# Kernel tuning notes

Hardware: AMD Instinct MI355X
Metric: run time of the kernel (lower is better)

## Reference

```python
import jax, jax.numpy as jnp
import numpy as np

N = 20000      # nodes
E = 160000     # edges
F_IN = 64      # node_feature_dim
HID = 256      # hidden_dim (= per-head out_channels, concat=False)
HEADS = 4
OUT = 2
BN_EPS = 1e-5


def setup_inputs() -> dict:
    key = jax.random.key(0)
    ks = jax.random.split(key, 24)
    s = 0.02

    def w(k, shape):
        return jax.random.normal(k, shape, jnp.float32) * s

    return {
        "node_feature": jax.random.normal(ks[0], (N, F_IN), jnp.float32),
        "edge_index": jax.random.randint(ks[1], (2, E), 0, N, jnp.int32),
        # layer 1 (in=F_IN)
        "wq1": w(ks[2], (F_IN, HEADS * HID)), "bq1": w(ks[3], (HEADS * HID,)),
        "wk1": w(ks[4], (F_IN, HEADS * HID)), "bk1": w(ks[5], (HEADS * HID,)),
        "wv1": w(ks[6], (F_IN, HEADS * HID)), "bv1": w(ks[7], (HEADS * HID,)),
        "ws1": w(ks[8], (F_IN, HID)),        "bs1": w(ks[9], (HID,)),
        # layer 2 (in=HID)
        "wq2": w(ks[10], (HID, HEADS * HID)), "bq2": w(ks[11], (HEADS * HID,)),
        "wk2": w(ks[12], (HID, HEADS * HID)), "bk2": w(ks[13], (HEADS * HID,)),
        "wv2": w(ks[14], (HID, HEADS * HID)), "bv2": w(ks[15], (HEADS * HID,)),
        "ws2": w(ks[16], (HID, HID)),         "bs2": w(ks[17], (HID,)),
        # batch norm affine
        "bn_gamma": jnp.ones((HID,), jnp.float32) + w(ks[18], (HID,)),
        "bn_beta": w(ks[19], (HID,)),
        # final linear
        "lin_w": w(ks[20], (HID, OUT)), "lin_b": w(ks[21], (OUT,)),
    }


def _transformer_conv(x, src, dst, wq, bq, wk, bk, wv, bv, ws, bs):
    """PyG TransformerConv, heads=HEADS, concat=False (mean over heads), root_weight."""
    n = x.shape[0]
    q = (x @ wq + bq).reshape(n, HEADS, HID)   # [N,H,C]
    k = (x @ wk + bk).reshape(n, HEADS, HID)
    v = (x @ wv + bv).reshape(n, HEADS, HID)
    # per-edge attention logits: q_i . k_j / sqrt(C)   (message j->i, i = dst)
    alpha = jnp.einsum('ehc,ehc->eh', q[dst], k[src]) / jnp.sqrt(jnp.float32(HID))  # [E,H]
    # scatter-softmax over incoming edges of each target node
    m = jax.ops.segment_max(alpha, dst, num_segments=n)
    m = jnp.where(jnp.isfinite(m), m, 0.0)  # nodes with no in-edges
    ex = jnp.exp(alpha - m[dst])
    denom = jax.ops.segment_sum(ex, dst, num_segments=n)
    a = ex / (denom[dst] + 1e-16)                          # [E,H]
    out = jax.ops.segment_sum(v[src] * a[..., None], dst, num_segments=n)  # [N,H,C]
    return out.mean(axis=1) + x @ ws + bs                  # concat=False -> head mean; + skip


def reference(node_feature, edge_index,
              wq1, bq1, wk1, bk1, wv1, bv1, ws1, bs1,
              wq2, bq2, wk2, bk2, wv2, bv2, ws2, bs2,
              bn_gamma, bn_beta, lin_w, lin_b):
    src, dst = edge_index[0], edge_index[1]
    x = _transformer_conv(node_feature, src, dst, wq1, bq1, wk1, bk1, wv1, bv1, ws1, bs1)
    x = _transformer_conv(x, src, dst, wq2, bq2, wk2, bk2, wv2, bv2, ws2, bs2)
    # BatchNorm1d (training mode: batch statistics, biased variance)
    mu = x.mean(axis=0)
    var = jnp.mean(jnp.square(x - mu), axis=0)
    x = bn_gamma * (x - mu) / jnp.sqrt(var + BN_EPS) + bn_beta
    rsu_embedding = x[0:1]                     # [1, HID]
    logits = jax.nn.relu(x @ lin_w + lin_b)    # [N, OUT]
    action_prob = jax.nn.softmax(logits, axis=1)
    return (action_prob, rsu_embedding)
```

## Files before the change

kernel.cpp:

```cpp
#include <hip/hip_runtime.h>
#include <hip/hip_bf16.h>
#include <math.h>

#define DI __device__ __forceinline__

constexpr int NN   = 20000;
constexpr int NE   = 160000;
constexpr int FIN  = 64;
constexpr int HIDC = 256;
constexpr int NH   = 4;
constexpr int NOUT = 3328;
constexpr int QKVW = 3072;
constexpr int CAPD = 128;

typedef __attribute__((ext_vector_type(8))) short short8;
typedef __attribute__((ext_vector_type(4))) float f32x4;
typedef __attribute__((ext_vector_type(2))) float f32x2;

DI float bf2f(unsigned short u) { return __uint_as_float(((unsigned)u) << 16); }

DI void gld16(const void* g, void* l) {
  __builtin_amdgcn_global_load_lds((const __attribute__((address_space(1))) unsigned*)g,
                                   (__attribute__((address_space(3))) unsigned*)l, 16, 0, 0);
}

DI unsigned fp8pack4(float a, float b, float c, float d) {
  int v = __builtin_amdgcn_cvt_pk_fp8_f32(a, b, 0, false);
  v = __builtin_amdgcn_cvt_pk_fp8_f32(c, d, v, true);
  return (unsigned)v;
}

__global__ void k_count(const int* __restrict__ dst, int* __restrict__ deg, int e_) {
  int e = blockIdx.x * blockDim.x + threadIdx.x;
  if (e < e_) atomicAdd(&deg[dst[e]], 1);
}

__global__ void k_scan(const int* __restrict__ deg, int* __restrict__ offs,
                       int* __restrict__ cursor, int n_) {
  __shared__ int part[1024];
  int tid = threadIdx.x;
  const int CH = (n_ + 1023) >> 10;
  int base = tid * CH;
  int s = 0;
  for (int i = 0; i < CH; ++i) { int idx = base + i; if (idx < n_) s += deg[idx]; }
  part[tid] = s;
  __syncthreads();
  for (int off = 1; off < 1024; off <<= 1) {
    int v = (tid >= off) ? part[tid - off] : 0;
    __syncthreads();
    part[tid] += v;
    __syncthreads();
  }
  int run = (tid == 0) ? 0 : part[tid - 1];
  for (int i = 0; i < CH; ++i) {
    int idx = base + i;
    if (idx < n_) { offs[idx] = run; cursor[idx] = run; run += deg[idx]; }
  }
  if (tid == 1023) offs[n_] = run;
}

__global__ void k_scatter(const int* __restrict__ dst, int* __restrict__ cursor,
                          int* __restrict__ eid, int e_) {
  int e = blockIdx.x * blockDim.x + threadIdx.x;
  if (e < e_) {
    int p = atomicAdd(&cursor[dst[e]], 1);
    eid[p] = e;
  }
}

__global__ void k_cast(const float* __restrict__ x, __hip_bfloat16* __restrict__ xb, int n) {
  int i = blockIdx.x * 256 + threadIdx.x;
  if (i < n) xb[i] = __float2bfloat16(x[i]);
}

template <int K>
__global__ void k_pack(const float* __restrict__ wq, const float* __restrict__ bq,
                       const float* __restrict__ wk, const float* __restrict__ bk,
                       const float* __restrict__ wv, const float* __restrict__ bv,
                       const float* __restrict__ ws, const float* __restrict__ bs,
                       __hip_bfloat16* __restrict__ Wt, float* __restrict__ biasp) {
  int n = blockIdx.x * 128 + threadIdx.x;
  int k = blockIdx.y;
  const float* w; const float* b; int off; int M;
  if (n < 1024)      { w = wq; b = bq; off = n;        M = 1024; }
  else if (n < 2048) { w = wk; b = bk; off = n - 1024; M = 1024; }
  else if (n < 3072) { w = wv; b = bv; off = n - 2048; M = 1024; }
  else               { w = ws; b = bs; off = n - 3072; M = 256;  }
  Wt[(size_t)n * K + k] = __float2bfloat16(w[(size_t)k * M + off]);
  if (k == 0) biasp[n] = b[off];
}

template <int K>
__global__ __launch_bounds__(256) void k_gemm_mfma(
    const __hip_bfloat16* __restrict__ X, const __hip_bfloat16* __restrict__ Wt,
    const float* __restrict__ biasp,
    __hip_bfloat16* __restrict__ qb, unsigned char* __restrict__ kb,
    unsigned char* __restrict__ vb, float* __restrict__ skip, int nrows,
    int RB, int CB) {
  __shared__ char lds[36864];
  const int tid = threadIdx.x;

  const int nwg = RB * CB;
  int bid = blockIdx.x;
  {
    int q8 = nwg >> 3, r8 = nwg & 7;
    int xcd = bid & 7, idx = bid >> 3;
    bid = (xcd < r8 ? xcd * (q8 + 1) : r8 * (q8 + 1) + (xcd - r8) * q8) + idx;
  }
  const int bm = (bid / CB) * 128;
  const int bn = (bid % CB) * 128;
  constexpr int KT = K / 32;

  const int srow = tid & 127;
  int ar = bm + srow; if (ar >= nrows) ar = nrows - 1;
  const int br = bn + srow;
  const int kb0 = (tid >> 7) * 8;
  const __hip_bfloat16* ax = X + (size_t)ar * K + kb0;
  const __hip_bfloat16* bx = Wt + (size_t)br * K + kb0;

  const int l = tid & 63, w = tid >> 6;
  const int wr = w >> 1, wc = w & 1;
  const int lm = l & 15, lk = l >> 4;
  const int aoff = (lk * 128 + wr * 64 + lm) * 16;
  const int boff = 8192 + (lk * 128 + wc * 64 + lm) * 16;

  f32x4 acc[4][4] = {};

  auto STAGE = [&](int buf, int kt) {
    char* base = lds + buf * 16384;
    const int ko = kt * 32;
    gld16(ax + ko,      base + tid * 16);
    gld16(ax + ko + 16, base + 4096 + tid * 16);
    gld16(bx + ko,      base + 8192 + tid * 16);
    gld16(bx + ko + 16, base + 12288 + tid * 16);
  };

  int cur = 0;
  STAGE(0, 0);
  __syncthreads();
#pragma unroll
  for (int kt = 0; kt < KT; ++kt) {
    if (kt + 1 < KT) STAGE(cur ^ 1, kt + 1);
    const char* base = lds + cur * 16384;
    short8 a[4], b[4];
#pragma unroll
    for (int m = 0; m < 4; ++m) a[m] = *(const short8*)(base + aoff + m * 256);
#pragma unroll
    for (int n = 0; n < 4; ++n) b[n] = *(const short8*)(base + boff + n * 256);
#pragma unroll
    for (int m = 0; m < 4; ++m)
#pragma unroll
      for (int n = 0; n < 4; ++n)
        acc[m][n] = __builtin_amdgcn_mfma_f32_16x16x32_bf16(a[m], b[n], acc[m][n], 0, 0, 0);
    __syncthreads();
    cur ^= 1;
  }

  if (bn < QKVW) {
    char* wb = lds + w * 9216;
    float bia[4];
#pragma unroll
    for (int n = 0; n < 4; ++n) bia[n] = biasp[bn + wc * 64 + n * 16 + lm];
#pragma unroll
    for (int m = 0; m < 4; ++m)
#pragma unroll
      for (int n = 0; n < 4; ++n)
#pragma unroll
        for (int r = 0; r < 4; ++r) {
          int rl = m * 16 + lk * 4 + r;
          int cl = n * 16 + lm;
          *(__hip_bfloat16*)(wb + rl * 144 + cl * 2) = __float2bfloat16(acc[m][n][r] + bia[n]);
        }
    __syncthreads();
    const int c8 = l & 7;
    const int r8 = l >> 3;
#pragma unroll
    for (int it = 0; it < 8; ++it) {
      int rl = it * 8 + r8;
      int grow = bm + wr * 64 + rl;
      if (grow >= nrows) continue;
      short8 t = *(const short8*)(wb + rl * 144 + c8 * 16);
      if (bn < 1024) {
        int col = bn + wc * 64 + c8 * 8;
        *(short8*)(qb + (size_t)grow * 1024 + col) = t;
      } else {
        float f0 = bf2f((unsigned short)t[0]), f1 = bf2f((unsigned short)t[1]);
        float f2 = bf2f((unsigned short)t[2]), f3 = bf2f((unsigned short)t[3]);
        float f4 = bf2f((unsigned short)t[4]), f5 = bf2f((unsigned short)t[5]);
        float f6 = bf2f((unsigned short)t[6]), f7 = bf2f((unsigned short)t[7]);
        uint2 d;
        d.x = fp8pack4(f0, f1, f2, f3);
        d.y = fp8pack4(f4, f5, f6, f7);
        if (bn < 2048) {
          int col = bn - 1024 + wc * 64 + c8 * 8;
          *(uint2*)(kb + (size_t)grow * 1024 + col) = d;
        } else {
          int col = bn - 2048 + wc * 64 + c8 * 8;
          *(uint2*)(vb + (size_t)grow * 1024 + col) = d;
        }
      }
    }
  } else {
    const int rbase = bm + wr * 64 + lk * 4;
    const int cb = bn + wc * 64 + lm;
#pragma unroll
    for (int n = 0; n < 4; ++n) {
      int col = cb + n * 16;
      float bia = biasp[col];
      int sc = col - QKVW;
#pragma unroll
      for (int m = 0; m < 4; ++m)
#pragma unroll
        for (int r = 0; r < 4; ++r) {
          int rr = rbase + m * 16 + r;
          if (rr < nrows) skip[(size_t)rr * HIDC + sc] = acc[m][n][r] + bia;
        }
    }
  }
}

__global__ __launch_bounds__(256) void k_attn(
    const __hip_bfloat16* __restrict__ qb, const unsigned char* __restrict__ kb,
    const unsigned char* __restrict__ vb,
    const int* __restrict__ offs, const int* __restrict__ eid,
    const int* __restrict__ src, float* __restrict__ xio,
    __hip_bfloat16* __restrict__ xb) {
  int n = blockIdx.x;
  int s0 = offs[n], s1 = offs[n + 1];
  int deg = s1 - s0;
  int tid = threadIdx.x;
  if (deg == 0) {
    if (xb != nullptr && tid < 64) {
      int c = tid * 4;
      const float* xr = xio + (size_t)n * HIDC;
#pragma unroll
      for (int j = 0; j < 4; ++j) xb[(size_t)n * HIDC + c + j] = __float2bfloat16(xr[c + j]);
    }
    return;
  }
  __shared__ int ses[CAPD];
  __shared__ float red[NH][HIDC];
  int h = tid >> 6, lane = tid & 63;
  int dc = deg < CAPD ? deg : CAPD;
  for (int i = tid; i < dc; i += 256) ses[i] = src[eid[s0 + i]];
  __syncthreads();

  const int hc = h * HIDC;
  int c = lane * 4;
  ushort4 q4 = *(const ushort4*)((const ushort*)qb + (size_t)n * 1024 + hc + c);
  float qx = bf2f(q4.x), qy = bf2f(q4.y), qz = bf2f(q4.z), qw = bf2f(q4.w);

  float denom = 0.f;
  float4 acc = make_float4(0.f, 0.f, 0.f, 0.f);
  for (int i = 0; i < deg; ++i) {
    int s = (i < CAPD) ? ses[i] : src[eid[s0 + i]];
    unsigned ku = *(const unsigned*)(kb + (size_t)s * 1024 + hc + c);
    unsigned vu = *(const unsigned*)(vb + (size_t)s * 1024 + hc + c);
    f32x2 k01 = __builtin_amdgcn_cvt_pk_f32_fp8(ku, false);
    f32x2 k23 = __builtin_amdgcn_cvt_pk_f32_fp8(ku, true);
    float p = qx * k01.x + qy * k01.y + qz * k23.x + qw * k23.y;
#pragma unroll
    for (int off = 32; off > 0; off >>= 1) p += __shfl_xor(p, off);
    float wgt = __expf(p * 0.0625f);
    denom += wgt;
    f32x2 v01 = __builtin_amdgcn_cvt_pk_f32_fp8(vu, false);
    f32x2 v23 = __builtin_amdgcn_cvt_pk_f32_fp8(vu, true);
    acc.x = fmaf(wgt, v01.x, acc.x);
    acc.y = fmaf(wgt, v01.y, acc.y);
    acc.z = fmaf(wgt, v23.x, acc.z);
    acc.w = fmaf(wgt, v23.y, acc.w);
  }
  float dinv = 1.f / (denom + 1e-16f);
  red[h][c + 0] = acc.x * dinv;
  red[h][c + 1] = acc.y * dinv;
  red[h][c + 2] = acc.z * dinv;
  red[h][c + 3] = acc.w * dinv;
  __syncthreads();
  if (tid < 64) {
    int c0 = tid * 4;
    float* xr = xio + (size_t)n * HIDC;
#pragma unroll
    for (int j = 0; j < 4; ++j) {
      float m = (red[0][c0 + j] + red[1][c0 + j] + red[2][c0 + j] + red[3][c0 + j]) * 0.25f;
      float val = m + xr[c0 + j];
      xr[c0 + j] = val;
      if (xb != nullptr) xb[(size_t)n * HIDC + c0 + j] = __float2bfloat16(val);
    }
  }
}

__global__ void k_bnstats(const float* __restrict__ x, float* __restrict__ sums,
                          float* __restrict__ sumsq, int n_) {
  int t = threadIdx.x;
  float s = 0.f, s2 = 0.f;
  for (int r = blockIdx.x; r < n_; r += gridDim.x) {
    float vv = x[(size_t)r * HIDC + t];
    s += vv; s2 += vv * vv;
  }
  atomicAdd(&sums[t], s);
  atomicAdd(&sumsq[t], s2);
}

__global__ void k_bnfin(const float* __restrict__ sums, const float* __restrict__ sumsq,
                        float* __restrict__ mu, float* __restrict__ rinv, int n_) {
  int t = threadIdx.x;
  float m = sums[t] / n_;
  float va = sumsq[t] / n_ - m * m;
  mu[t] = m;
  rinv[t] = 1.f / sqrtf(fmaxf(va, 0.f) + 1e-5f);
}

__global__ __launch_bounds__(64) void k_final(
    const float* __restrict__ x, const float* __restrict__ mu, const float* __restrict__ rinv,
    const float* __restrict__ gamma, const float* __restrict__ beta,
    const float* __restrict__ lw, const float* __restrict__ lb,
    float* __restrict__ out, int n_) {
  int n = blockIdx.x;
  int lane = threadIdx.x;
  int c = lane * 4;
  const float* xr = x + (size_t)n * HIDC;
  float4 xv = *(const float4*)(xr + c);
  float4 muv = *(const float4*)(mu + c);
  float4 rv  = *(const float4*)(rinv + c);
  float4 gv  = *(const float4*)(gamma + c);
  float4 bv  = *(const float4*)(beta + c);
  float y0 = gv.x * (xv.x - muv.x) * rv.x + bv.x;
  float y1 = gv.y * (xv.y - muv.y) * rv.y + bv.y;
  float y2 = gv.z * (xv.z - muv.z) * rv.z + bv.z;
  float y3 = gv.w * (xv.w - muv.w) * rv.w + bv.w;
  float4 wa = *(const float4*)(lw + (size_t)c * 2);
  float4 wb = *(const float4*)(lw + (size_t)c * 2 + 4);
  float p0 = y0 * wa.x + y1 * wa.z + y2 * wb.x + y3 * wb.z;
  float p1 = y0 * wa.y + y1 * wa.w + y2 * wb.y + y3 * wb.w;
#pragma unroll
  for (int off = 32; off > 0; off >>= 1) {
    p0 += __shfl_xor(p0, off);
    p1 += __shfl_xor(p1, off);
  }
  if (n == 0) *(float4*)(out + (size_t)NN * 2 + c) = make_float4(y0, y1, y2, y3);
  if (lane == 0) {
    float l0 = fmaxf(p0 + lb[0], 0.f);
    float l1 = fmaxf(p1 + lb[1], 0.f);
    float m = fmaxf(l0, l1);
    float e0 = expf(l0 - m), e1 = expf(l1 - m);
    float inv = 1.f / (e0 + e1);
    out[(size_t)n * 2 + 0] = e0 * inv;
    out[(size_t)n * 2 + 1] = e1 * inv;
  }
}

extern "C" void kernel_launch(void* const* d_in, const int* in_sizes, int n_in,
                              void* d_out, int out_size, void* d_ws, size_t ws_size,
                              hipStream_t stream) {
  const float* x0  = (const float*)d_in[0];
  const int*   ei  = (const int*)d_in[1];
  const float* wq1 = (const float*)d_in[2];  const float* bq1 = (const float*)d_in[3];
  const float* wk1 = (const float*)d_in[4];  const float* bk1 = (const float*)d_in[5];
  const float* wv1 = (const float*)d_in[6];  const float* bv1 = (const float*)d_in[7];
  const float* ws1 = (const float*)d_in[8];  const float* bs1 = (const float*)d_in[9];
  const float* wq2 = (const float*)d_in[10]; const float* bq2 = (const float*)d_in[11];
  const float* wk2 = (const float*)d_in[12]; const float* bk2 = (const float*)d_in[13];
  const float* wv2 = (const float*)d_in[14]; const float* bv2 = (const float*)d_in[15];
  const float* ws2 = (const float*)d_in[16]; const float* bs2 = (const float*)d_in[17];
  const float* gam = (const float*)d_in[18]; const float* bet = (const float*)d_in[19];
  const float* lw  = (const float*)d_in[20]; const float* lb  = (const float*)d_in[21];
  const int* srcv = ei;
  const int* dstv = ei + NE;

  char* p = (char*)d_ws;
  auto take = [&](size_t bytes) {
    char* r = p;
    p += (bytes + 255) & ~(size_t)255;
    return r;
  };
  __hip_bfloat16* qb = (__hip_bfloat16*)take((size_t)NN * 1024 * 2);
  unsigned char* kbuf = (unsigned char*)take((size_t)NN * 1024);
  unsigned char* vbuf = (unsigned char*)take((size_t)NN * 1024);
  __hip_bfloat16* x0b = (__hip_bfloat16*)take((size_t)NN * FIN * 2);
  __hip_bfloat16* x2b = (__hip_bfloat16*)take((size_t)NN * HIDC * 2);
  __hip_bfloat16* Wt  = (__hip_bfloat16*)take((size_t)NOUT * HIDC * 2);
  float* x2    = (float*)take((size_t)NN * HIDC * 4);
  float* x3    = (float*)take((size_t)NN * HIDC * 4);
  float* biasp = (float*)take((size_t)NOUT * 4);
  float* bnbuf = (float*)take(4 * HIDC * 4);
  int* deg    = (int*)take((size_t)NN * 4);
  int* offs   = (int*)take((size_t)(NN + 1) * 4);
  int* cursor = (int*)take((size_t)NN * 4);
  int* eidb   = (int*)take((size_t)NE * 4);
  if ((size_t)(p - (char*)d_ws) > ws_size) return;

  float* sums  = bnbuf;
  float* sumsq = bnbuf + HIDC;
  float* mu    = bnbuf + 2 * HIDC;
  float* rinv  = bnbuf + 3 * HIDC;

  hipMemsetAsync(deg, 0, (size_t)NN * 4, stream);
  hipMemsetAsync(bnbuf, 0, 2 * HIDC * 4, stream);
  k_count<<<(NE + 255) / 256, 256, 0, stream>>>(dstv, deg, NE);
  k_scan<<<1, 1024, 0, stream>>>(deg, offs, cursor, NN);
  k_scatter<<<(NE + 255) / 256, 256, 0, stream>>>(dstv, cursor, eidb, NE);
  k_cast<<<(NN * FIN + 255) / 256, 256, 0, stream>>>(x0, x0b, NN * FIN);

  const int RB = (NN + 127) / 128;
  const int CB = NOUT / 128;
  k_pack<FIN><<<dim3(CB, FIN), 128, 0, stream>>>(wq1, bq1, wk1, bk1, wv1, bv1, ws1, bs1, Wt, biasp);
  k_gemm_mfma<FIN><<<RB * CB, 256, 0, stream>>>(x0b, Wt, biasp, qb, kbuf, vbuf, x2, NN, RB, CB);
  k_attn<<<NN, 256, 0, stream>>>(qb, kbuf, vbuf, offs, eidb, srcv, x2, x2b);
  k_pack<HIDC><<<dim3(CB, HIDC), 128, 0, stream>>>(wq2, bq2, wk2, bk2, wv2, bv2, ws2, bs2, Wt, biasp);
  k_gemm_mfma<HIDC><<<RB * CB, 256, 0, stream>>>(x2b, Wt, biasp, qb, kbuf, vbuf, x3, NN, RB, CB);
  k_attn<<<NN, 256, 0, stream>>>(qb, kbuf, vbuf, offs, eidb, srcv, x3, nullptr);
  k_bnstats<<<256, 256, 0, stream>>>(x3, sums, sumsq, NN);
  k_bnfin<<<1, HIDC, 0, stream>>>(sums, sumsq, mu, rinv, NN);
  k_final<<<NN, 64, 0, stream>>>(x3, mu, rinv, gam, bet, lw, lb, (float*)d_out, NN);
}
```

Before: 413.5 us.

## Load GEMM operands directly to registers, store Q in fp8, fuse small kernels

```diff
diff --git a/kernel.cpp b/kernel.cpp
--- a/kernel.cpp
+++ b/kernel.cpp
@@ -10,7 +10,6 @@
 constexpr int HIDC = 256;
 constexpr int NH   = 4;
 constexpr int NOUT = 3328;
-constexpr int QKVW = 3072;
 constexpr int CAPD = 128;
 
 typedef __attribute__((ext_vector_type(8))) short short8;
@@ -18,11 +17,6 @@
 typedef __attribute__((ext_vector_type(2))) float f32x2;
 
 DI float bf2f(unsigned short u) { return __uint_as_float(((unsigned)u) << 16); }
-
-DI void gld16(const void* g, void* l) {
-  __builtin_amdgcn_global_load_lds((const __attribute__((address_space(1))) unsigned*)g,
-                                   (__attribute__((address_space(3))) unsigned*)l, 16, 0, 0);
-}
 
 DI unsigned fp8pack4(float a, float b, float c, float d) {
   int v = __builtin_amdgcn_cvt_pk_fp8_f32(a, b, 0, false);
@@ -30,9 +24,11 @@
   return (unsigned)v;
 }
 
-__global__ void k_count(const int* __restrict__ dst, int* __restrict__ deg, int e_) {
-  int e = blockIdx.x * blockDim.x + threadIdx.x;
-  if (e < e_) atomicAdd(&deg[dst[e]], 1);
+__global__ void k_prep(const float* __restrict__ x, __hip_bfloat16* __restrict__ xb,
+                       const int* __restrict__ dst, int* __restrict__ deg) {
+  int gid = blockIdx.x * 256 + threadIdx.x;
+  if (gid < NN * FIN) xb[gid] = __float2bfloat16(x[gid]);
+  if (gid < NE) atomicAdd(&deg[dst[gid]], 1);
 }
 
 __global__ void k_scan(const int* __restrict__ deg, int* __restrict__ offs,
@@ -68,11 +64,6 @@
   }
 }
 
-__global__ void k_cast(const float* __restrict__ x, __hip_bfloat16* __restrict__ xb, int n) {
-  int i = blockIdx.x * 256 + threadIdx.x;
-  if (i < n) xb[i] = __float2bfloat16(x[i]);
-}
-
 template <int K>
 __global__ void k_pack(const float* __restrict__ wq, const float* __restrict__ bq,
                        const float* __restrict__ wk, const float* __restrict__ bk,
@@ -91,13 +82,13 @@
 }
 
 template <int K>
-__global__ __launch_bounds__(256) void k_gemm_mfma(
+__global__ __launch_bounds__(256) void k_gemm_reg(
     const __hip_bfloat16* __restrict__ X, const __hip_bfloat16* __restrict__ Wt,
     const float* __restrict__ biasp,
-    __hip_bfloat16* __restrict__ qb, unsigned char* __restrict__ kb,
-    unsigned char* __restrict__ vb, float* __restrict__ skip, int nrows,
-    int RB, int CB) {
-  __shared__ char lds[36864];
+    unsigned char* __restrict__ qb, unsigned char* __restrict__ kb,
+    unsigned char* __restrict__ vb, __hip_bfloat16* __restrict__ skipb,
+    int nrows, int RB, int CB) {
+  __shared__ char eplds[36864];
   const int tid = threadIdx.x;
 
   const int nwg = RB * CB;
@@ -111,130 +102,98 @@
   const int bn = (bid % CB) * 128;
   constexpr int KT = K / 32;
 
-  const int srow = tid & 127;
-  int ar = bm + srow; if (ar >= nrows) ar = nrows - 1;
-  const int br = bn + srow;
-  const int kb0 = (tid >> 7) * 8;
-  const __hip_bfloat16* ax = X + (size_t)ar * K + kb0;
-  const __hip_bfloat16* bx = Wt + (size_t)br * K + kb0;
-
   const int l = tid & 63, w = tid >> 6;
   const int wr = w >> 1, wc = w & 1;
   const int lm = l & 15, lk = l >> 4;
-  const int aoff = (lk * 128 + wr * 64 + lm) * 16;
-  const int boff = 8192 + (lk * 128 + wc * 64 + lm) * 16;
+
+  const __hip_bfloat16* Ap[4];
+  const __hip_bfloat16* Bp[4];
+#pragma unroll
+  for (int m = 0; m < 4; ++m) {
+    int row = bm + wr * 64 + m * 16 + lm;
+    if (row >= nrows) row = nrows - 1;
+    Ap[m] = X + (size_t)row * K + lk * 8;
+  }
+#pragma unroll
+  for (int n = 0; n < 4; ++n) {
+    int col = bn + wc * 64 + n * 16 + lm;
+    Bp[n] = Wt + (size_t)col * K + lk * 8;
+  }
 
   f32x4 acc[4][4] = {};
-
-  auto STAGE = [&](int buf, int kt) {
-    char* base = lds + buf * 16384;
-    const int ko = kt * 32;
-    gld16(ax + ko,      base + tid * 16);
-    gld16(ax + ko + 16, base + 4096 + tid * 16);
-    gld16(bx + ko,      base + 8192 + tid * 16);
-    gld16(bx + ko + 16, base + 12288 + tid * 16);
-  };
-
-  int cur = 0;
-  STAGE(0, 0);
-  __syncthreads();
-#pragma unroll
+#pragma unroll 2
   for (int kt = 0; kt < KT; ++kt) {
-    if (kt + 1 < KT) STAGE(cur ^ 1, kt + 1);
-    const char* base = lds + cur * 16384;
     short8 a[4], b[4];
 #pragma unroll
-    for (int m = 0; m < 4; ++m) a[m] = *(const short8*)(base + aoff + m * 256);
-#pragma unroll
-    for (int n = 0; n < 4; ++n) b[n] = *(const short8*)(base + boff + n * 256);
+    for (int m = 0; m < 4; ++m) a[m] = *(const short8*)(Ap[m] + kt * 32);
+#pragma unroll
+    for (int n = 0; n < 4; ++n) b[n] = *(const short8*)(Bp[n] + kt * 32);
 #pragma unroll
     for (int m = 0; m < 4; ++m)
 #pragma unroll
       for (int n = 0; n < 4; ++n)
         acc[m][n] = __builtin_amdgcn_mfma_f32_16x16x32_bf16(a[m], b[n], acc[m][n], 0, 0, 0);
-    __syncthreads();
-    cur ^= 1;
-  }
-
-  if (bn < QKVW) {
-    char* wb = lds + w * 9216;
-    float bia[4];
-#pragma unroll
-    for (int n = 0; n < 4; ++n) bia[n] = biasp[bn + wc * 64 + n * 16 + lm];
-#pragma unroll
-    for (int m = 0; m < 4; ++m)
-#pragma unroll
-      for (int n = 0; n < 4; ++n)
-#pragma unroll
-        for (int r = 0; r < 4; ++r) {
-          int rl = m * 16 + lk * 4 + r;
-          int cl = n * 16 + lm;
-          *(__hip_bfloat16*)(wb + rl * 144 + cl * 2) = __float2bfloat16(acc[m][n][r] + bia[n]);
-        }
-    __syncthreads();
-    const int c8 = l & 7;
-    const int r8 = l >> 3;
-#pragma unroll
-    for (int it = 0; it < 8; ++it) {
-      int rl = it * 8 + r8;
-      int grow = bm + wr * 64 + rl;
-      if (grow >= nrows) continue;
-      short8 t = *(const short8*)(wb + rl * 144 + c8 * 16);
-      if (bn < 1024) {
-        int col = bn + wc * 64 + c8 * 8;
-        *(short8*)(qb + (size_t)grow * 1024 + col) = t;
-      } else {
-        float f0 = bf2f((unsigned short)t[0]), f1 = bf2f((unsigned short)t[1]);
-        float f2 = bf2f((unsigned short)t[2]), f3 = bf2f((unsigned short)t[3]);
-        float f4 = bf2f((unsigned short)t[4]), f5 = bf2f((unsigned short)t[5]);
-        float f6 = bf2f((unsigned short)t[6]), f7 = bf2f((unsigned short)t[7]);
-        uint2 d;
-        d.x = fp8pack4(f0, f1, f2, f3);
-        d.y = fp8pack4(f4, f5, f6, f7);
-        if (bn < 2048) {
-          int col = bn - 1024 + wc * 64 + c8 * 8;
-          *(uint2*)(kb + (size_t)grow * 1024 + col) = d;
-        } else {
-          int col = bn - 2048 + wc * 64 + c8 * 8;
-          *(uint2*)(vb + (size_t)grow * 1024 + col) = d;
-        }
+  }
+
+  char* ep = eplds + w * 9216;
+  float bia[4];
+#pragma unroll
+  for (int n = 0; n < 4; ++n) bia[n] = biasp[bn + wc * 64 + n * 16 + lm];
+#pragma unroll
+  for (int m = 0; m < 4; ++m)
+#pragma unroll
+    for (int n = 0; n < 4; ++n)
+#pragma unroll
+      for (int r = 0; r < 4; ++r) {
+        int rl = m * 16 + lk * 4 + r;
+        int cl = n * 16 + lm;
+        *(__hip_bfloat16*)(ep + rl * 144 + cl * 2) = __float2bfloat16(acc[m][n][r] + bia[n]);
       }
+  const int c8 = l & 7;
+  const int r8 = l >> 3;
+#pragma unroll
+  for (int it = 0; it < 8; ++it) {
+    int rl = it * 8 + r8;
+    int grow = bm + wr * 64 + rl;
+    if (grow >= nrows) continue;
+    short8 t = *(const short8*)(ep + rl * 144 + c8 * 16);
+    int colg = bn + wc * 64 + c8 * 8;
+    if (colg < 3072) {
+      float f0 = bf2f((unsigned short)t[0]), f1 = bf2f((unsigned short)t[1]);
+      float f2 = bf2f((unsigned short)t[2]), f3 = bf2f((unsigned short)t[3]);
+      float f4 = bf2f((unsigned short)t[4]), f5 = bf2f((unsigned short)t[5]);
+      float f6 = bf2f((unsigned short)t[6]), f7 = bf2f((unsigned short)t[7]);
+      uint2 d;
+      d.x = fp8pack4(f0, f1, f2, f3);
+      d.y = fp8pack4(f4, f5, f6, f7);
+      if (colg < 1024)      *(uint2*)(qb + (size_t)grow * 1024 + colg)        = d;
+      else if (colg < 2048) *(uint2*)(kb + (size_t)grow * 1024 + colg - 1024) = d;
+      else                  *(uint2*)(vb + (size_t)grow * 1024 + colg - 2048) = d;
+    } else {
+      *(short8*)((__hip_bfloat16*)skipb + (size_t)grow * HIDC + colg - 3072) = t;
     }
-  } else {
-    const int rbase = bm + wr * 64 + lk * 4;
-    const int cb = bn + wc * 64 + lm;
-#pragma unroll
-    for (int n = 0; n < 4; ++n) {
-      int col = cb + n * 16;
-      float bia = biasp[col];
-      int sc = col - QKVW;
-#pragma unroll
-      for (int m = 0; m < 4; ++m)
-#pragma unroll
-        for (int r = 0; r < 4; ++r) {
-          int rr = rbase + m * 16 + r;
-          if (rr < nrows) skip[(size_t)rr * HIDC + sc] = acc[m][n][r] + bia;
-        }
-    }
   }
 }
 
 __global__ __launch_bounds__(256) void k_attn(
-    const __hip_bfloat16* __restrict__ qb, const unsigned char* __restrict__ kb,
+    const unsigned char* __restrict__ qb, const unsigned char* __restrict__ kb,
     const unsigned char* __restrict__ vb,
     const int* __restrict__ offs, const int* __restrict__ eid,
-    const int* __restrict__ src, float* __restrict__ xio,
-    __hip_bfloat16* __restrict__ xb) {
+    const int* __restrict__ src, const __hip_bfloat16* __restrict__ skipb,
+    __hip_bfloat16* __restrict__ outb, float* __restrict__ outf) {
   int n = blockIdx.x;
   int s0 = offs[n], s1 = offs[n + 1];
   int deg = s1 - s0;
   int tid = threadIdx.x;
   if (deg == 0) {
-    if (xb != nullptr && tid < 64) {
+    if (tid < 64) {
       int c = tid * 4;
-      const float* xr = xio + (size_t)n * HIDC;
-#pragma unroll
-      for (int j = 0; j < 4; ++j) xb[(size_t)n * HIDC + c + j] = __float2bfloat16(xr[c + j]);
+      ushort4 sv = *(const ushort4*)((const ushort*)skipb + (size_t)n * HIDC + c);
+      if (outb != nullptr) *(ushort4*)((ushort*)outb + (size_t)n * HIDC + c) = sv;
+      if (outf != nullptr) {
+        float* xr = outf + (size_t)n * HIDC + c;
+        xr[0] = bf2f(sv.x); xr[1] = bf2f(sv.y); xr[2] = bf2f(sv.z); xr[3] = bf2f(sv.w);
+      }
     }
     return;
   }
@@ -247,28 +206,37 @@
 
   const int hc = h * HIDC;
   int c = lane * 4;
-  ushort4 q4 = *(const ushort4*)((const ushort*)qb + (size_t)n * 1024 + hc + c);
-  float qx = bf2f(q4.x), qy = bf2f(q4.y), qz = bf2f(q4.z), qw = bf2f(q4.w);
+  unsigned qu = *(const unsigned*)(qb + (size_t)n * 1024 + hc + c);
+  f32x2 q01 = __builtin_amdgcn_cvt_pk_f32_fp8(qu, false);
+  f32x2 q23 = __builtin_amdgcn_cvt_pk_f32_fp8(qu, true);
+  float qx = q01.x, qy = q01.y, qz = q23.x, qw = q23.y;
 
   float denom = 0.f;
   float4 acc = make_float4(0.f, 0.f, 0.f, 0.f);
+  int sc0 = ses[0];
+  unsigned ku0 = *(const unsigned*)(kb + (size_t)sc0 * 1024 + hc + c);
+  unsigned vu0 = *(const unsigned*)(vb + (size_t)sc0 * 1024 + hc + c);
   for (int i = 0; i < deg; ++i) {
-    int s = (i < CAPD) ? ses[i] : src[eid[s0 + i]];
-    unsigned ku = *(const unsigned*)(kb + (size_t)s * 1024 + hc + c);
-    unsigned vu = *(const unsigned*)(vb + (size_t)s * 1024 + hc + c);
-    f32x2 k01 = __builtin_amdgcn_cvt_pk_f32_fp8(ku, false);
-    f32x2 k23 = __builtin_amdgcn_cvt_pk_f32_fp8(ku, true);
+    unsigned ku1 = 0, vu1 = 0;
+    if (i + 1 < deg) {
+      int s1i = (i + 1 < CAPD) ? ses[i + 1] : src[eid[s0 + i + 1]];
+      ku1 = *(const unsigned*)(kb + (size_t)s1i * 1024 + hc + c);
+      vu1 = *(const unsigned*)(vb + (size_t)s1i * 1024 + hc + c);
+    }
+    f32x2 k01 = __builtin_amdgcn_cvt_pk_f32_fp8(ku0, false);
+    f32x2 k23 = __builtin_amdgcn_cvt_pk_f32_fp8(ku0, true);
     float p = qx * k01.x + qy * k01.y + qz * k23.x + qw * k23.y;
 #pragma unroll
     for (int off = 32; off > 0; off >>= 1) p += __shfl_xor(p, off);
     float wgt = __expf(p * 0.0625f);
     denom += wgt;
-    f32x2 v01 = __builtin_amdgcn_cvt_pk_f32_fp8(vu, false);
-    f32x2 v23 = __builtin_amdgcn_cvt_pk_f32_fp8(vu, true);
+    f32x2 v01 = __builtin_amdgcn_cvt_pk_f32_fp8(vu0, false);
+    f32x2 v23 = __builtin_amdgcn_cvt_pk_f32_fp8(vu0, true);
     acc.x = fmaf(wgt, v01.x, acc.x);
     acc.y = fmaf(wgt, v01.y, acc.y);
     acc.z = fmaf(wgt, v23.x, acc.z);
     acc.w = fmaf(wgt, v23.y, acc.w);
+    ku0 = ku1; vu0 = vu1;
   }
   float dinv = 1.f / (denom + 1e-16f);
   red[h][c + 0] = acc.x * dinv;
@@ -278,13 +246,14 @@
   __syncthreads();
   if (tid < 64) {
     int c0 = tid * 4;
-    float* xr = xio + (size_t)n * HIDC;
+    ushort4 sv = *(const ushort4*)((const ushort*)skipb + (size_t)n * HIDC + c0);
+    float sk[4] = {bf2f(sv.x), bf2f(sv.y), bf2f(sv.z), bf2f(sv.w)};
 #pragma unroll
     for (int j = 0; j < 4; ++j) {
       float m = (red[0][c0 + j] + red[1][c0 + j] + red[2][c0 + j] + red[3][c0 + j]) * 0.25f;
-      float val = m + xr[c0 + j];
-      xr[c0 + j] = val;
-      if (xb != nullptr) xb[(size_t)n * HIDC + c0 + j] = __float2bfloat16(val);
+      float val = m + sk[j];
+      if (outb != nullptr) ((ushort*)outb)[(size_t)n * HIDC + c0 + j] = (ushort)(__bfloat16_as_ushort(__float2bfloat16(val)));
+      if (outf != nullptr) outf[(size_t)n * HIDC + c0 + j] = val;
     }
   }
 }
@@ -301,33 +270,31 @@
   atomicAdd(&sumsq[t], s2);
 }
 
-__global__ void k_bnfin(const float* __restrict__ sums, const float* __restrict__ sumsq,
-                        float* __restrict__ mu, float* __restrict__ rinv, int n_) {
-  int t = threadIdx.x;
-  float m = sums[t] / n_;
-  float va = sumsq[t] / n_ - m * m;
-  mu[t] = m;
-  rinv[t] = 1.f / sqrtf(fmaxf(va, 0.f) + 1e-5f);
-}
-
-__global__ __launch_bounds__(64) void k_final(
-    const float* __restrict__ x, const float* __restrict__ mu, const float* __restrict__ rinv,
+__global__ __launch_bounds__(256) void k_final(
+    const float* __restrict__ x, const float* __restrict__ sums, const float* __restrict__ sumsq,
     const float* __restrict__ gamma, const float* __restrict__ beta,
     const float* __restrict__ lw, const float* __restrict__ lb,
     float* __restrict__ out, int n_) {
-  int n = blockIdx.x;
-  int lane = threadIdx.x;
+  int sub = threadIdx.x >> 6, lane = threadIdx.x & 63;
+  int n = blockIdx.x * 4 + sub;
+  if (n >= n_) return;
   int c = lane * 4;
+  float4 sm  = *(const float4*)(sums + c);
+  float4 sq  = *(const float4*)(sumsq + c);
+  const float inv_n = 1.f / (float)n_;
+  float mu0 = sm.x * inv_n, mu1 = sm.y * inv_n, mu2 = sm.z * inv_n, mu3 = sm.w * inv_n;
+  float r0 = 1.f / sqrtf(fmaxf(sq.x * inv_n - mu0 * mu0, 0.f) + 1e-5f);
+  float r1 = 1.f / sqrtf(fmaxf(sq.y * inv_n - mu1 * mu1, 0.f) + 1e-5f);
+  float r2 = 1.f / sqrtf(fmaxf(sq.z * inv_n - mu2 * mu2, 0.f) + 1e-5f);
+  float r3 = 1.f / sqrtf(fmaxf(sq.w * inv_n - mu3 * mu3, 0.f) + 1e-5f);
   const float* xr = x + (size_t)n * HIDC;
   float4 xv = *(const float4*)(xr + c);
-  float4 muv = *(const float4*)(mu + c);
-  float4 rv  = *(const float4*)(rinv + c);
-  float4 gv  = *(const float4*)(gamma + c);
-  float4 bv  = *(const float4*)(beta + c);
-  float y0 = gv.x * (xv.x - muv.x) * rv.x + bv.x;
-  float y1 = gv.y * (xv.y - muv.y) * rv.y + bv.y;
-  float y2 = gv.z * (xv.z - muv.z) * rv.z + bv.z;
-  float y3 = gv.w * (xv.w - muv.w) * rv.w + bv.w;
+  float4 gv = *(const float4*)(gamma + c);
+  float4 bv = *(const float4*)(beta + c);
+  float y0 = gv.x * (xv.x - mu0) * r0 + bv.x;
+  float y1 = gv.y * (xv.y - mu1) * r1 + bv.y;
+  float y2 = gv.z * (xv.z - mu2) * r2 + bv.z;
+  float y3 = gv.w * (xv.w - mu3) * r3 + bv.w;
   float4 wa = *(const float4*)(lw + (size_t)c * 2);
   float4 wb = *(const float4*)(lw + (size_t)c * 2 + 4);
   float p0 = y0 * wa.x + y1 * wa.z + y2 * wb.x + y3 * wb.z;
@@ -373,16 +340,16 @@
     p += (bytes + 255) & ~(size_t)255;
     return r;
   };
-  __hip_bfloat16* qb = (__hip_bfloat16*)take((size_t)NN * 1024 * 2);
+  unsigned char* qbuf = (unsigned char*)take((size_t)NN * 1024);
   unsigned char* kbuf = (unsigned char*)take((size_t)NN * 1024);
   unsigned char* vbuf = (unsigned char*)take((size_t)NN * 1024);
+  __hip_bfloat16* skipb = (__hip_bfloat16*)take((size_t)NN * HIDC * 2);
   __hip_bfloat16* x0b = (__hip_bfloat16*)take((size_t)NN * FIN * 2);
   __hip_bfloat16* x2b = (__hip_bfloat16*)take((size_t)NN * HIDC * 2);
   __hip_bfloat16* Wt  = (__hip_bfloat16*)take((size_t)NOUT * HIDC * 2);
-  float* x2    = (float*)take((size_t)NN * HIDC * 4);
   float* x3    = (float*)take((size_t)NN * HIDC * 4);
   float* biasp = (float*)take((size_t)NOUT * 4);
-  float* bnbuf = (float*)take(4 * HIDC * 4);
+  float* bnbuf = (float*)take(2 * HIDC * 4);
   int* deg    = (int*)take((size_t)NN * 4);
   int* offs   = (int*)take((size_t)(NN + 1) * 4);
   int* cursor = (int*)take((size_t)NN * 4);
@@ -391,25 +358,21 @@
 
   float* sums  = bnbuf;
   float* sumsq = bnbuf + HIDC;
-  float* mu    = bnbuf + 2 * HIDC;
-  float* rinv  = bnbuf + 3 * HIDC;
 
   hipMemsetAsync(deg, 0, (size_t)NN * 4, stream);
   hipMemsetAsync(bnbuf, 0, 2 * HIDC * 4, stream);
-  k_count<<<(NE + 255) / 256, 256, 0, stream>>>(dstv, deg, NE);
+  k_prep<<<(NN * FIN + 255) / 256, 256, 0, stream>>>(x0, x0b, dstv, deg);
   k_scan<<<1, 1024, 0, stream>>>(deg, offs, cursor, NN);
   k_scatter<<<(NE + 255) / 256, 256, 0, stream>>>(dstv, cursor, eidb, NE);
-  k_cast<<<(NN * FIN + 255) / 256, 256, 0, stream>>>(x0, x0b, NN * FIN);
 
   const int RB = (NN + 127) / 128;
   const int CB = NOUT / 128;
   k_pack<FIN><<<dim3(CB, FIN), 128, 0, stream>>>(wq1, bq1, wk1, bk1, wv1, bv1, ws1, bs1, Wt, biasp);
-  k_gemm_mfma<FIN><<<RB * CB, 256, 0, stream>>>(x0b, Wt, biasp, qb, kbuf, vbuf, x2, NN, RB, CB);
-  k_attn<<<NN, 256, 0, stream>>>(qb, kbuf, vbuf, offs, eidb, srcv, x2, x2b);
+  k_gemm_reg<FIN><<<RB * CB, 256, 0, stream>>>(x0b, Wt, biasp, qbuf, kbuf, vbuf, skipb, NN, RB, CB);
+  k_attn<<<NN, 256, 0, stream>>>(qbuf, kbuf, vbuf, offs, eidb, srcv, skipb, x2b, nullptr);
   k_pack<HIDC><<<dim3(CB, HIDC), 128, 0, stream>>>(wq2, bq2, wk2, bk2, wv2, bv2, ws2, bs2, Wt, biasp);
-  k_gemm_mfma<HIDC><<<RB * CB, 256, 0, stream>>>(x2b, Wt, biasp, qb, kbuf, vbuf, x3, NN, RB, CB);
-  k_attn<<<NN, 256, 0, stream>>>(qb, kbuf, vbuf, offs, eidb, srcv, x3, nullptr);
+  k_gemm_reg<HIDC><<<RB * CB, 256, 0, stream>>>(x2b, Wt, biasp, qbuf, kbuf, vbuf, skipb, NN, RB, CB);
+  k_attn<<<NN, 256, 0, stream>>>(qbuf, kbuf, vbuf, offs, eidb, srcv, skipb, nullptr, x3);
   k_bnstats<<<256, 256, 0, stream>>>(x3, sums, sumsq, NN);
-  k_bnfin<<<1, HIDC, 0, stream>>>(sums, sumsq, mu, rinv, NN);
-  k_final<<<NN, 64, 0, stream>>>(x3, mu, rinv, gam, bet, lw, lb, (float*)d_out, NN);
-}
+  k_final<<<(NN + 3) / 4, 256, 0, stream>>>(x3, sums, sumsq, gam, bet, lw, lb, (float*)d_out, NN);
+}
```

Measured after the change: 434.9 us. +5.2%, slower.
